# Kernel tuning notes

Hardware: AMD Instinct MI355X
Metric: run time of the kernel (lower is better)

## Reference

```python
import jax, jax.numpy as jnp
import numpy as np

N_TOKENS, D_MODEL, D_FF, N_EXPERTS, TOP_K = 4096, 2048, 1408, 8, 2


def setup_inputs() -> dict:
    key = jax.random.key(0)
    ks = jax.random.split(key, 6)
    s = 0.02
    return {
        "x": jax.random.normal(ks[0], (N_TOKENS, D_MODEL), jnp.float32),
        "topK_indices": jax.random.randint(ks[1], (N_TOKENS, TOP_K), 0, N_EXPERTS, jnp.int32),
        "topK_scores": jax.random.uniform(ks[2], (N_TOKENS, TOP_K), jnp.float32),
        "W_gate": jax.random.normal(ks[3], (N_EXPERTS, D_MODEL, D_FF), jnp.float32) * s,
        "W_up": jax.random.normal(ks[4], (N_EXPERTS, D_MODEL, D_FF), jnp.float32) * s,
        "W_down": jax.random.normal(ks[5], (N_EXPERTS, D_FF, D_MODEL), jnp.float32) * s,
    }


def reference(x, topK_indices, topK_scores, W_gate, W_up, W_down):
    # Combine weights: combine[n, e] = sum over k of score[n, k] where idx[n, k] == e.
    # Mathematically identical to the torch sort/split/index_add dispatch-combine
    # (with multiply_gate_scores=True), expressed densely for a clean jax baseline.
    n = x.shape[0]
    rows = jnp.arange(n)[:, None]  # [N, 1]
    combine = jnp.zeros((n, W_gate.shape[0]), x.dtype).at[rows, topK_indices].add(topK_scores)
    # Per-expert SwiGLU MLP (llama-moe LinearGLUExperts, bias-free).
    h = jax.nn.silu(jnp.einsum("nd,edh->enh", x, W_gate)) * jnp.einsum("nd,edh->enh", x, W_up)
    expert_out = jnp.einsum("enh,ehd->end", h, W_down)  # [E, N, D]
    y = jnp.einsum("ne,end->nd", combine, expert_out)  # weighted scatter-add combine
    return y
```

## Files before the change

kernel.cpp:

```cpp
#include <hip/hip_runtime.h>
#include <hip/hip_bf16.h>


#define NTOK 4096
#define DMODEL 2048
#define DFF 1408
#define NEXP 8
#define TOPK 2
#define NSLOT (NTOK * TOPK)
#define MAX_TILES 160
#define NTILE_A 40
#define NTILE_B 72
#define NY1 11
#define NY2 16

typedef short bf16x8 __attribute__((ext_vector_type(8)));
typedef float f32x4 __attribute__((ext_vector_type(4)));

#define MFMA16(a, b, c) __builtin_amdgcn_mfma_f32_16x16x32_bf16(a, b, c, 0, 0, 0)

__device__ inline void async16(const void* g, void* l) {
    __builtin_amdgcn_global_load_lds(
        (const __attribute__((address_space(1))) void*)g,
        (__attribute__((address_space(3))) void*)l, 16, 0, 0);
}

__device__ inline int xcd_swz(int bid, int nblk) {
    int q = nblk >> 3, r = nblk & 7;
    int x = bid & 7, p = bid >> 3;
    return (x < r ? x * (q + 1) : r * (q + 1) + (x - r) * q) + p;
}

__global__ __launch_bounds__(256) void route_kernel(
    const int* __restrict__ idx, const float* __restrict__ scores,
    int* __restrict__ metaA, int* __restrict__ metaB,
    int* __restrict__ slot_token, float* __restrict__ slot_score,
    int* __restrict__ tok_slot, int bmA, int bmB)
{
    __shared__ int counts[NEXP];
    __shared__ int cursor[NEXP];
    int t = threadIdx.x;
    if (t < NEXP) counts[t] = 0;
    __syncthreads();
    for (int i = t; i < NSLOT; i += 256) atomicAdd(&counts[idx[i]], 1);
    __syncthreads();
    if (t == 0) {
        int off = 0, nt = 0;
        for (int e = 0; e < NEXP; e++) {
            cursor[e] = off;
            int c = counts[e];
            for (int s = 0; s < c && nt < MAX_TILES; s += bmA) {
                metaA[1 + nt * 3 + 0] = e;
                metaA[1 + nt * 3 + 1] = off + s;
                metaA[1 + nt * 3 + 2] = min(bmA, c - s);
                nt++;
            }
            off += c;
        }
        metaA[0] = nt;
        off = 0; nt = 0;
        for (int e = 0; e < NEXP; e++) {
            int c = counts[e];
            for (int s = 0; s < c && nt < MAX_TILES; s += bmB) {
                metaB[1 + nt * 3 + 0] = e;
                metaB[1 + nt * 3 + 1] = off + s;
                metaB[1 + nt * 3 + 2] = min(bmB, c - s);
                nt++;
            }
            off += c;
        }
        metaB[0] = nt;
    }
    __syncthreads();
    for (int i = t; i < NSLOT; i += 256) {
        int e = idx[i];
        int pos = atomicAdd(&cursor[e], 1);
        slot_token[pos] = i / TOPK;
        slot_score[pos] = scores[i];
        tok_slot[i] = pos;
    }
}

__global__ __launch_bounds__(256) void convert_x(
    const float* __restrict__ x, __hip_bfloat16* __restrict__ xb)
{
    int i = blockIdx.x * 256 + threadIdx.x;
    float4 v = reinterpret_cast<const float4*>(x)[i];
    __hip_bfloat16 o[4] = {(__hip_bfloat16)v.x, (__hip_bfloat16)v.y,
                           (__hip_bfloat16)v.z, (__hip_bfloat16)v.w};
    *reinterpret_cast<uint2*>(&xb[(size_t)i * 4]) = *reinterpret_cast<uint2*>(o);
}

__global__ __launch_bounds__(256) void transpose_convert(
    const float* __restrict__ in, __hip_bfloat16* __restrict__ out, int R, int C)
{
    __shared__ __hip_bfloat16 t[64][72];
    const size_t base = (size_t)blockIdx.z * R * C;
    const int c0 = blockIdx.x * 64, r0 = blockIdx.y * 64;
    const int tid = threadIdx.x;
    const int rl = tid >> 4, c4 = (tid & 15) * 4;
    #pragma unroll
    for (int j = 0; j < 4; j++) {
        int r = rl + j * 16;
        float4 v = *reinterpret_cast<const float4*>(&in[base + (size_t)(r0 + r) * C + c0 + c4]);
        t[c4 + 0][r] = (__hip_bfloat16)v.x;
        t[c4 + 1][r] = (__hip_bfloat16)v.y;
        t[c4 + 2][r] = (__hip_bfloat16)v.z;
        t[c4 + 3][r] = (__hip_bfloat16)v.w;
    }
    __syncthreads();
    const int nl = tid >> 3, k8 = (tid & 7) * 8;
    #pragma unroll
    for (int j = 0; j < 2; j++) {
        int n = nl + j * 32;
        const uint* p = reinterpret_cast<const uint*>(&t[n][k8]);
        uint4 o = {p[0], p[1], p[2], p[3]};
        *reinterpret_cast<uint4*>(&out[base + (size_t)(c0 + n) * R + r0 + k8]) = o;
    }
}

__global__ __launch_bounds__(256) void combine_kernel(
    const __hip_bfloat16* __restrict__ so, const int* __restrict__ tok_slot,
    const float* __restrict__ slot_score, float* __restrict__ out)
{
    const int tok = blockIdx.x;
    const int c = threadIdx.x * 8;
    const int s0 = tok_slot[tok * 2 + 0], s1 = tok_slot[tok * 2 + 1];
    const float w0 = slot_score[s0], w1 = slot_score[s1];
    bf16x8 v0 = *reinterpret_cast<const bf16x8*>(&so[(size_t)s0 * DMODEL + c]);
    bf16x8 v1 = *reinterpret_cast<const bf16x8*>(&so[(size_t)s1 * DMODEL + c]);
    float res[8];
    #pragma unroll
    for (int j = 0; j < 8; j++) {
        float f0 = __uint_as_float(((uint)(unsigned short)v0[j]) << 16);
        float f1 = __uint_as_float(((uint)(unsigned short)v1[j]) << 16);
        res[j] = w0 * f0 + w1 * f1;
    }
    float4* dst = reinterpret_cast<float4*>(&out[(size_t)tok * DMODEL + c]);
    dst[0] = *reinterpret_cast<float4*>(&res[0]);
    dst[1] = *reinterpret_cast<float4*>(&res[4]);
}

__global__ __launch_bounds__(512, 2) void moe_gemm1_fast(
    const __hip_bfloat16* __restrict__ xb,
    const __hip_bfloat16* __restrict__ WgT, const __hip_bfloat16* __restrict__ WuT,
    const int* __restrict__ meta, const int* __restrict__ slot_token,
    __hip_bfloat16* __restrict__ h)
{
    const int swz = xcd_swz(blockIdx.x, NTILE_A * NY1);
    const int tile = swz / NY1, yb = swz % NY1;
    if (tile >= meta[0]) return;
    const int e = meta[1 + tile * 3], slot0 = meta[2 + tile * 3], rows = meta[3 + tile * 3];
    const int n0 = yb * 128;

    __shared__ __hip_bfloat16 As[2][256][64];
    __shared__ __hip_bfloat16 Bgs[2][128][64];
    __shared__ __hip_bfloat16 Bus[2][128][64];

    const int tid = threadIdx.x, lane = tid & 63, w = tid >> 6;
    const int wm = w >> 2, wn = w & 3, l15 = lane & 15, lg = lane >> 4;
    const int swb = l15 & 7;

    uint aoff[4], boff[2];
    #pragma unroll
    for (int i = 0; i < 4; i++) {
        int chunk = tid + i * 512;
        int r = chunk >> 3;
        int rc = r < rows ? r : rows - 1;
        int slot8 = (chunk & 7) ^ (r & 7);
        aoff[i] = (uint)(slot_token[slot0 + rc] * (DMODEL * 2) + slot8 * 16);
    }
    #pragma unroll
    for (int i = 0; i < 2; i++) {
        int chunk = tid + i * 512;
        int n = chunk >> 3;
        int slot8 = (chunk & 7) ^ (n & 7);
        boff[i] = (uint)((n0 + n) * (DMODEL * 2) + slot8 * 16);
    }
    const char* xbp = (const char*)xb;
    const char* wgp = (const char*)(WgT + (size_t)e * DFF * DMODEL);
    const char* wup = (const char*)(WuT + (size_t)e * DFF * DMODEL);

    f32x4 ag[8][2] = {};
    f32x4 au[8][2] = {};

    auto stage = [&](int kt, int buf) {
        const int kb = kt * 128;
        char* ab = (char*)As[buf]  + w * 1024;
        char* gb = (char*)Bgs[buf] + w * 1024;
        char* ub = (char*)Bus[buf] + w * 1024;
        #pragma unroll
        for (int i = 0; i < 4; i++) async16(xbp + aoff[i] + kb, ab + i * 8192);
        #pragma unroll
        for (int i = 0; i < 2; i++) {
            async16(wgp + boff[i] + kb, gb + i * 8192);
            async16(wup + boff[i] + kb, ub + i * 8192);
        }
    };

    constexpr int NT = DMODEL / 64;
    stage(0, 0);
    stage(1, 1);

    for (int kt = 0; kt < NT; ++kt) {
        const int cur = kt & 1;
        if (kt < NT - 1) asm volatile("s_waitcnt vmcnt(8)" ::: "memory");
        else             asm volatile("s_waitcnt vmcnt(0)" ::: "memory");
        __builtin_amdgcn_s_barrier();

        bf16x8 bgk[2], buk[2];
        #pragma unroll
        for (int p = 0; p < 4; p++) {
            const int kk = p >> 1, mh = p & 1;
            const int cb = ((kk * 4 + lg) ^ swb) * 16;
            bf16x8 a[4];
            #pragma unroll
            for (int mi = 0; mi < 4; mi++)
                a[mi] = *(const bf16x8*)((const char*)&As[cur][wm * 128 + (mh * 4 + mi) * 16 + l15][0] + cb);
            if (mh == 0) {
                #pragma unroll
                for (int nf = 0; nf < 2; nf++) {
                    bgk[nf] = *(const bf16x8*)((const char*)&Bgs[cur][wn * 32 + nf * 16 + l15][0] + cb);
                    buk[nf] = *(const bf16x8*)((const char*)&Bus[cur][wn * 32 + nf * 16 + l15][0] + cb);
                }
            }
            asm volatile("s_waitcnt lgkmcnt(0)" ::: "memory");
            __builtin_amdgcn_sched_barrier(0);
            __builtin_amdgcn_s_setprio(1);
            #pragma unroll
            for (int mi = 0; mi < 4; mi++) {
                const int mf = mh * 4 + mi;
                #pragma unroll
                for (int nf = 0; nf < 2; nf++) {
                    ag[mf][nf] = MFMA16(a[mi], bgk[nf], ag[mf][nf]);
                    au[mf][nf] = MFMA16(a[mi], buk[nf], au[mf][nf]);
                }
            }
            __builtin_amdgcn_s_setprio(0);
            __builtin_amdgcn_s_barrier();
        }
        if (kt + 2 < NT) stage(kt + 2, cur);
    }

    #pragma unroll
    for (int mf = 0; mf < 8; mf++) {
        #pragma unroll
        for (int j = 0; j < 4; j++) {
            int r = wm * 128 + mf * 16 + lg * 4 + j;
            if (r < rows) {
                size_t hrow = (size_t)(slot0 + r) * DFF + n0 + wn * 32;
                #pragma unroll
                for (int nf = 0; nf < 2; nf++) {
                    float g = ag[mf][nf][j], u = au[mf][nf][j];
                    float hv = g / (1.0f + __expf(-g)) * u;
                    h[hrow + nf * 16 + l15] = (__hip_bfloat16)hv;
                }
            }
        }
    }
}

__global__ __launch_bounds__(256, 2) void moe_gemm2_fast(
    const __hip_bfloat16* __restrict__ h, const __hip_bfloat16* __restrict__ WdT,
    const int* __restrict__ meta, __hip_bfloat16* __restrict__ so)
{
    const int swz = xcd_swz(blockIdx.x, NTILE_B * NY2);
    const int tile = swz / NY2, yb = swz % NY2;
    if (tile >= meta[0]) return;
    const int e = meta[1 + tile * 3], slot0 = meta[2 + tile * 3], rows = meta[3 + tile * 3];
    const int n0 = yb * 128;

    __shared__ __hip_bfloat16 Ah[2][128][64];
    __shared__ __hip_bfloat16 Bd[2][128][64];

    const int tid = threadIdx.x, lane = tid & 63, w = tid >> 6;
    const int wm = w >> 1, wn = w & 1, l15 = lane & 15, lg = lane >> 4;
    const int swb = l15 & 7;

    uint aoff[4], boff[4];
    #pragma unroll
    for (int i = 0; i < 4; i++) {
        int chunk = tid + i * 256;
        int r = chunk >> 3;
        int rc = r < rows ? r : rows - 1;
        int slot8 = (chunk & 7) ^ (r & 7);
        aoff[i] = (uint)((slot0 + rc) * (DFF * 2) + slot8 * 16);
        boff[i] = (uint)((n0 + r) * (DFF * 2) + slot8 * 16);
    }
    const char* hp  = (const char*)h;
    const char* wdp = (const char*)(WdT + (size_t)e * DMODEL * DFF);

    f32x4 acc[4][4] = {};

    auto stage = [&](int kt, int buf) {
        const int kb = kt * 128;
        char* ab = (char*)Ah[buf] + w * 1024;
        char* bb = (char*)Bd[buf] + w * 1024;
        #pragma unroll
        for (int i = 0; i < 4; i++) {
            async16(hp  + aoff[i] + kb, ab + i * 4096);
            async16(wdp + boff[i] + kb, bb + i * 4096);
        }
    };

    constexpr int NT = DFF / 64;
    stage(0, 0);
    stage(1, 1);

    for (int kt = 0; kt < NT; ++kt) {
        const int cur = kt & 1;
        if (kt < NT - 1) asm volatile("s_waitcnt vmcnt(8)" ::: "memory");
        else             asm volatile("s_waitcnt vmcnt(0)" ::: "memory");
        __builtin_amdgcn_s_barrier();

        #pragma unroll
        for (int p = 0; p < 2; p++) {
            const int cb = ((p * 4 + lg) ^ swb) * 16;
            bf16x8 a[4], b[4];
            #pragma unroll
            for (int mf = 0; mf < 4; mf++) {
                a[mf] = *(const bf16x8*)((const char*)&Ah[cur][wm * 64 + mf * 16 + l15][0] + cb);
                b[mf] = *(const bf16x8*)((const char*)&Bd[cur][wn * 64 + mf * 16 + l15][0] + cb);
            }
            asm volatile("s_waitcnt lgkmcnt(0)" ::: "memory");
            __builtin_amdgcn_sched_barrier(0);
            __builtin_amdgcn_s_setprio(1);
            #pragma unroll
            for (int mf = 0; mf < 4; mf++)
                #pragma unroll
                for (int nf = 0; nf < 4; nf++)
                    acc[mf][nf] = MFMA16(a[mf], b[nf], acc[mf][nf]);
            __builtin_amdgcn_s_setprio(0);
            __builtin_amdgcn_s_barrier();
        }
        if (kt + 2 < NT) stage(kt + 2, cur);
    }

    #pragma unroll
    for (int mf = 0; mf < 4; mf++) {
        #pragma unroll
        for (int j = 0; j < 4; j++) {
            int r = wm * 64 + mf * 16 + lg * 4 + j;
            if (r < rows) {
                size_t orow = (size_t)(slot0 + r) * DMODEL + n0 + wn * 64;
                #pragma unroll
                for (int nf = 0; nf < 4; nf++)
                    so[orow + nf * 16 + l15] = (__hip_bfloat16)acc[mf][nf][j];
            }
        }
    }
}

__global__ __launch_bounds__(256) void moe_gemm1(
    const float* __restrict__ x, const float* __restrict__ Wg, const float* __restrict__ Wu,
    const int* __restrict__ meta, const int* __restrict__ slot_token,
    __hip_bfloat16* __restrict__ h)
{
    int tile = blockIdx.x;
    if (tile >= meta[0]) return;
    const int e = meta[1 + tile * 3], slot0 = meta[2 + tile * 3], rows = meta[3 + tile * 3];
    const int n0 = blockIdx.y * 64;
    __shared__ __hip_bfloat16 As[64][72];
    __shared__ __hip_bfloat16 Bgs[64][72];
    __shared__ __hip_bfloat16 Bus[64][72];
    const int tid = threadIdx.x, lane = tid & 63, w = tid >> 6;
    const int wm = w >> 1, wn = w & 1, l15 = lane & 15, lg = lane >> 4;
    const float* __restrict__ WgE = Wg + (size_t)e * DMODEL * DFF;
    const float* __restrict__ WuE = Wu + (size_t)e * DMODEL * DFF;
    f32x4 acc_g[2][2] = {};
    f32x4 acc_u[2][2] = {};
    for (int k0 = 0; k0 < DMODEL; k0 += 64) {
        __syncthreads();
        #pragma unroll
        for (int j = 0; j < 4; j++) {
            int linear = tid + j * 256;
            int r = linear >> 4, c4 = (linear & 15) * 4;
            int tok = (r < rows) ? slot_token[slot0 + r] : 0;
            float4 v = *reinterpret_cast<const float4*>(&x[(size_t)tok * DMODEL + k0 + c4]);
            As[r][c4 + 0] = (__hip_bfloat16)v.x; As[r][c4 + 1] = (__hip_bfloat16)v.y;
            As[r][c4 + 2] = (__hip_bfloat16)v.z; As[r][c4 + 3] = (__hip_bfloat16)v.w;
        }
        #pragma unroll
        for (int j = 0; j < 4; j++) {
            int linear = tid + j * 256;
            int k = linear >> 4, n4 = (linear & 15) * 4;
            float4 vg = *reinterpret_cast<const float4*>(&WgE[(size_t)(k0 + k) * DFF + n0 + n4]);
            Bgs[n4 + 0][k] = (__hip_bfloat16)vg.x; Bgs[n4 + 1][k] = (__hip_bfloat16)vg.y;
            Bgs[n4 + 2][k] = (__hip_bfloat16)vg.z; Bgs[n4 + 3][k] = (__hip_bfloat16)vg.w;
            float4 vu = *reinterpret_cast<const float4*>(&WuE[(size_t)(k0 + k) * DFF + n0 + n4]);
            Bus[n4 + 0][k] = (__hip_bfloat16)vu.x; Bus[n4 + 1][k] = (__hip_bfloat16)vu.y;
            Bus[n4 + 2][k] = (__hip_bfloat16)vu.z; Bus[n4 + 3][k] = (__hip_bfloat16)vu.w;
        }
        __syncthreads();
        #pragma unroll
        for (int kk = 0; kk < 2; kk++) {
            bf16x8 a[2], bg[2], bu[2];
            #pragma unroll
            for (int mf = 0; mf < 2; mf++)
                a[mf] = *reinterpret_cast<const bf16x8*>(&As[wm * 32 + mf * 16 + l15][kk * 32 + lg * 8]);
            #pragma unroll
            for (int nf = 0; nf < 2; nf++) {
                bg[nf] = *reinterpret_cast<const bf16x8*>(&Bgs[wn * 32 + nf * 16 + l15][kk * 32 + lg * 8]);
                bu[nf] = *reinterpret_cast<const bf16x8*>(&Bus[wn * 32 + nf * 16 + l15][kk * 32 + lg * 8]);
            }
            #pragma unroll
            for (int mf = 0; mf < 2; mf++)
                #pragma unroll
                for (int nf = 0; nf < 2; nf++) {
                    acc_g[mf][nf] = MFMA16(a[mf], bg[nf], acc_g[mf][nf]);
                    acc_u[mf][nf] = MFMA16(a[mf], bu[nf], acc_u[mf][nf]);
                }
        }
    }
    #pragma unroll
    for (int mf = 0; mf < 2; mf++)
        #pragma unroll
        for (int nf = 0; nf < 2; nf++)
            #pragma unroll
            for (int j = 0; j < 4; j++) {
                int r = wm * 32 + mf * 16 + lg * 4 + j;
                int c = wn * 32 + nf * 16 + l15;
                if (r < rows) {
                    float g = acc_g[mf][nf][j], u = acc_u[mf][nf][j];
                    h[(size_t)(slot0 + r) * DFF + n0 + c] = (__hip_bfloat16)(g / (1.0f + __expf(-g)) * u);
                }
            }
}

__global__ __launch_bounds__(256) void moe_gemm2(
    const __hip_bfloat16* __restrict__ h, const float* __restrict__ Wd,
    const int* __restrict__ meta, const int* __restrict__ slot_token,
    const float* __restrict__ slot_score, float* __restrict__ out)
{
    int tile = blockIdx.x;
    if (tile >= meta[0]) return;
    const int e = meta[1 + tile * 3], slot0 = meta[2 + tile * 3], rows = meta[3 + tile * 3];
    const int n0 = blockIdx.y * 64;
    __shared__ __hip_bfloat16 As[64][72];
    __shared__ __hip_bfloat16 Bs[64][72];
    const int tid = threadIdx.x, lane = tid & 63, w = tid >> 6;
    const int wm = w >> 1, wn = w & 1, l15 = lane & 15, lg = lane >> 4;
    const float* __restrict__ WdE = Wd + (size_t)e * DFF * DMODEL;
    f32x4 acc[2][2] = {};
    for (int k0 = 0; k0 < DFF; k0 += 64) {
        __syncthreads();
        #pragma unroll
        for (int j = 0; j < 2; j++) {
            int linear = tid + j * 256;
            int r = linear >> 3, c8 = (linear & 7) * 8;
            bf16x8 v = *reinterpret_cast<const bf16x8*>(&h[(size_t)(slot0 + r) * DFF + k0 + c8]);
            *reinterpret_cast<bf16x8*>(&As[r][c8]) = v;
        }
        #pragma unroll
        for (int j = 0; j < 4; j++) {
            int linear = tid + j * 256;
            int k = linear >> 4, n4 = (linear & 15) * 4;
            float4 v = *reinterpret_cast<const float4*>(&WdE[(size_t)(k0 + k) * DMODEL + n0 + n4]);
            Bs[n4 + 0][k] = (__hip_bfloat16)v.x; Bs[n4 + 1][k] = (__hip_bfloat16)v.y;
            Bs[n4 + 2][k] = (__hip_bfloat16)v.z; Bs[n4 + 3][k] = (__hip_bfloat16)v.w;
        }
        __syncthreads();
        #pragma unroll
        for (int kk = 0; kk < 2; kk++) {
            bf16x8 a[2], b[2];
            #pragma unroll
            for (int mf = 0; mf < 2; mf++)
                a[mf] = *reinterpret_cast<const bf16x8*>(&As[wm * 32 + mf * 16 + l15][kk * 32 + lg * 8]);
            #pragma unroll
            for (int nf = 0; nf < 2; nf++)
                b[nf] = *reinterpret_cast<const bf16x8*>(&Bs[wn * 32 + nf * 16 + l15][kk * 32 + lg * 8]);
            #pragma unroll
            for (int mf = 0; mf < 2; mf++)
                #pragma unroll
                for (int nf = 0; nf < 2; nf++)
                    acc[mf][nf] = MFMA16(a[mf], b[nf], acc[mf][nf]);
        }
    }
    #pragma unroll
    for (int mf = 0; mf < 2; mf++)
        #pragma unroll
        for (int nf = 0; nf < 2; nf++)
            #pragma unroll
            for (int j = 0; j < 4; j++) {
                int r = wm * 32 + mf * 16 + lg * 4 + j;
                int c = wn * 32 + nf * 16 + l15;
                if (r < rows) {
                    int slot = slot0 + r;
                    atomicAdd(&out[(size_t)slot_token[slot] * DMODEL + n0 + c],
                              acc[mf][nf][j] * slot_score[slot]);
                }
            }
}

extern "C" void kernel_launch(void* const* d_in, const int* in_sizes, int n_in,
                              void* d_out, int out_size, void* d_ws, size_t ws_size,
                              hipStream_t stream) {
    const float* x      = (const float*)d_in[0];
    const int*   idx    = (const int*)d_in[1];
    const float* scores = (const float*)d_in[2];
    const float* Wg     = (const float*)d_in[3];
    const float* Wu     = (const float*)d_in[4];
    const float* Wd     = (const float*)d_in[5];
    float* out = (float*)d_out;

    char* ws = (char*)d_ws;
    int*   metaA      = (int*)ws;
    int*   metaB      = (int*)(ws + 4096);
    int*   slot_token = (int*)(ws + 8192);
    float* slot_score = (float*)(ws + 8192 + 40960);
    int*   tok_slot   = (int*)(ws + 8192 + 81920);

    const size_t XB_OFF = (size_t)1 << 20;
    const size_t HB_OFF = (size_t)20 << 20;
    const size_t WG_OFF = (size_t)44 << 20;
    const size_t WU_OFF = (size_t)92 << 20;
    const size_t WD_OFF = (size_t)140 << 20;
    const size_t NEED   = (size_t)187 << 20;
    const bool fast = ws_size >= NEED;

    route_kernel<<<1, 256, 0, stream>>>(idx, scores, metaA, metaB, slot_token, slot_score,
                                        tok_slot, fast ? 256 : 64, fast ? 128 : 64);

    if (fast) {
        __hip_bfloat16* xb  = (__hip_bfloat16*)(ws + XB_OFF);
        __hip_bfloat16* hb  = (__hip_bfloat16*)(ws + HB_OFF);
        __hip_bfloat16* WgT = (__hip_bfloat16*)(ws + WG_OFF);
        __hip_bfloat16* WuT = (__hip_bfloat16*)(ws + WU_OFF);
        __hip_bfloat16* WdT = (__hip_bfloat16*)(ws + WD_OFF);
        __hip_bfloat16* sot = (__hip_bfloat16*)(ws + WG_OFF);

        dim3 td(DMODEL / 64, DFF / 64, NEXP);
        transpose_convert<<<td, 256, 0, stream>>>(Wd, WdT, DFF, DMODEL);
        dim3 tg(DFF / 64, DMODEL / 64, NEXP);
        transpose_convert<<<tg, 256, 0, stream>>>(Wg, WgT, DMODEL, DFF);
        transpose_convert<<<tg, 256, 0, stream>>>(Wu, WuT, DMODEL, DFF);
        convert_x<<<(NTOK * DMODEL / 4) / 256, 256, 0, stream>>>(x, xb);

        moe_gemm1_fast<<<NTILE_A * NY1, 512, 0, stream>>>(xb, WgT, WuT, metaA, slot_token, hb);
        moe_gemm2_fast<<<NTILE_B * NY2, 256, 0, stream>>>(hb, WdT, metaB, sot);
        combine_kernel<<<NTOK, 256, 0, stream>>>(sot, tok_slot, slot_score, out);
    } else {
        __hip_bfloat16* hb = (__hip_bfloat16*)(ws + HB_OFF);
        hipMemsetAsync(d_out, 0, (size_t)NTOK * DMODEL * sizeof(float), stream);
        dim3 g1(NSLOT / 64 + NEXP, DFF / 64);
        moe_gemm1<<<g1, 256, 0, stream>>>(x, Wg, Wu, metaA, slot_token, hb);
        dim3 g2(NSLOT / 64 + NEXP, DMODEL / 64);
        moe_gemm2<<<g2, 256, 0, stream>>>(hb, Wd, metaB, slot_token, slot_score, out);
    }
}
```

Before: 364.6 us.

## Restructure MoE GEMM main loops to issue next-stage loads before final MFMAs

In the fused gate/up GEMM, the per-k-tile loop is split into four MFMA phases: gate and up for the first 64 rows, then gate and up for the last 64 rows. The B fragments are kept in registers, and the async global-to-LDS prefetch of tile kt+2 is issued before the final up-projection MFMA batch so that it overlaps with compute. In the down GEMM, all LDS fragments for the tile are loaded at once, the prefetch is issued immediately after a single barrier, and all MFMAs then run. This cuts the barriers per k-tile and overlaps the next stage's loads with compute, at the cost of more fragment registers and changed barrier placement that must keep the LDS double-buffer safe.

```diff
diff --git a/kernel.cpp b/kernel.cpp
--- a/kernel.cpp
+++ b/kernel.cpp
@@ -208,45 +208,91 @@
         else             asm volatile("s_waitcnt vmcnt(0)" ::: "memory");
         __builtin_amdgcn_s_barrier();
 
-        bf16x8 bgk[2], buk[2];
-        #pragma unroll
-        for (int p = 0; p < 4; p++) {
-            const int kk = p >> 1, mh = p & 1;
+        bf16x8 a[4][2], bg[2][2], bu[2][2];
+
+        #pragma unroll
+        for (int kk = 0; kk < 2; kk++) {
             const int cb = ((kk * 4 + lg) ^ swb) * 16;
-            bf16x8 a[4];
             #pragma unroll
             for (int mi = 0; mi < 4; mi++)
-                a[mi] = *(const bf16x8*)((const char*)&As[cur][wm * 128 + (mh * 4 + mi) * 16 + l15][0] + cb);
-            if (mh == 0) {
-                #pragma unroll
-                for (int nf = 0; nf < 2; nf++) {
-                    bgk[nf] = *(const bf16x8*)((const char*)&Bgs[cur][wn * 32 + nf * 16 + l15][0] + cb);
-                    buk[nf] = *(const bf16x8*)((const char*)&Bus[cur][wn * 32 + nf * 16 + l15][0] + cb);
-                }
-            }
-            asm volatile("s_waitcnt lgkmcnt(0)" ::: "memory");
-            __builtin_amdgcn_sched_barrier(0);
-            __builtin_amdgcn_s_setprio(1);
-            #pragma unroll
-            for (int mi = 0; mi < 4; mi++) {
-                const int mf = mh * 4 + mi;
-                #pragma unroll
-                for (int nf = 0; nf < 2; nf++) {
-                    ag[mf][nf] = MFMA16(a[mi], bgk[nf], ag[mf][nf]);
-                    au[mf][nf] = MFMA16(a[mi], buk[nf], au[mf][nf]);
-                }
-            }
-            __builtin_amdgcn_s_setprio(0);
-            __builtin_amdgcn_s_barrier();
-        }
+                a[mi][kk] = *(const bf16x8*)((const char*)&As[cur][wm * 128 + mi * 16 + l15][0] + cb);
+            #pragma unroll
+            for (int nf = 0; nf < 2; nf++)
+                bg[nf][kk] = *(const bf16x8*)((const char*)&Bgs[cur][wn * 32 + nf * 16 + l15][0] + cb);
+        }
+        __builtin_amdgcn_s_barrier();
+        asm volatile("s_waitcnt lgkmcnt(0)" ::: "memory");
+        __builtin_amdgcn_sched_barrier(0);
+        __builtin_amdgcn_s_setprio(1);
+        #pragma unroll
+        for (int kk = 0; kk < 2; kk++)
+            #pragma unroll
+            for (int mi = 0; mi < 4; mi++)
+                #pragma unroll
+                for (int nf = 0; nf < 2; nf++)
+                    ag[mi][nf] = MFMA16(a[mi][kk], bg[nf][kk], ag[mi][nf]);
+        __builtin_amdgcn_s_setprio(0);
+        __builtin_amdgcn_s_barrier();
+
+        #pragma unroll
+        for (int kk = 0; kk < 2; kk++) {
+            const int cb = ((kk * 4 + lg) ^ swb) * 16;
+            #pragma unroll
+            for (int nf = 0; nf < 2; nf++)
+                bu[nf][kk] = *(const bf16x8*)((const char*)&Bus[cur][wn * 32 + nf * 16 + l15][0] + cb);
+        }
+        __builtin_amdgcn_s_barrier();
+        asm volatile("s_waitcnt lgkmcnt(0)" ::: "memory");
+        __builtin_amdgcn_sched_barrier(0);
+        __builtin_amdgcn_s_setprio(1);
+        #pragma unroll
+        for (int kk = 0; kk < 2; kk++)
+            #pragma unroll
+            for (int mi = 0; mi < 4; mi++)
+                #pragma unroll
+                for (int nf = 0; nf < 2; nf++)
+                    au[mi][nf] = MFMA16(a[mi][kk], bu[nf][kk], au[mi][nf]);
+        __builtin_amdgcn_s_setprio(0);
+        __builtin_amdgcn_s_barrier();
+
+        #pragma unroll
+        for (int kk = 0; kk < 2; kk++) {
+            const int cb = ((kk * 4 + lg) ^ swb) * 16;
+            #pragma unroll
+            for (int mi = 0; mi < 4; mi++)
+                a[mi][kk] = *(const bf16x8*)((const char*)&As[cur][wm * 128 + 64 + mi * 16 + l15][0] + cb);
+        }
+        __builtin_amdgcn_s_barrier();
+        asm volatile("s_waitcnt lgkmcnt(0)" ::: "memory");
+        __builtin_amdgcn_sched_barrier(0);
+        __builtin_amdgcn_s_setprio(1);
+        #pragma unroll
+        for (int kk = 0; kk < 2; kk++)
+            #pragma unroll
+            for (int mi = 0; mi < 4; mi++)
+                #pragma unroll
+                for (int nf = 0; nf < 2; nf++)
+                    ag[4 + mi][nf] = MFMA16(a[mi][kk], bg[nf][kk], ag[4 + mi][nf]);
+        __builtin_amdgcn_s_setprio(0);
+        __builtin_amdgcn_s_barrier();
+
         if (kt + 2 < NT) stage(kt + 2, cur);
+        __builtin_amdgcn_s_setprio(1);
+        #pragma unroll
+        for (int kk = 0; kk < 2; kk++)
+            #pragma unroll
+            for (int mi = 0; mi < 4; mi++)
+                #pragma unroll
+                for (int nf = 0; nf < 2; nf++)
+                    au[4 + mi][nf] = MFMA16(a[mi][kk], bu[nf][kk], au[4 + mi][nf]);
+        __builtin_amdgcn_s_setprio(0);
     }
 
     #pragma unroll
     for (int mf = 0; mf < 8; mf++) {
         #pragma unroll
         for (int j = 0; j < 4; j++) {
-            int r = wm * 128 + mf * 16 + lg * 4 + j;
+            int r = wm * 128 + ((mf >> 2) * 64) + (mf & 3) * 16 + lg * 4 + j;
             if (r < rows) {
                 size_t hrow = (size_t)(slot0 + r) * DFF + n0 + wn * 32;
                 #pragma unroll
@@ -313,27 +359,30 @@
         else             asm volatile("s_waitcnt vmcnt(0)" ::: "memory");
         __builtin_amdgcn_s_barrier();
 
-        #pragma unroll
-        for (int p = 0; p < 2; p++) {
-            const int cb = ((p * 4 + lg) ^ swb) * 16;
-            bf16x8 a[4], b[4];
+        bf16x8 a[2][4], b[2][4];
+        #pragma unroll
+        for (int kk = 0; kk < 2; kk++) {
+            const int cb = ((kk * 4 + lg) ^ swb) * 16;
             #pragma unroll
             for (int mf = 0; mf < 4; mf++) {
-                a[mf] = *(const bf16x8*)((const char*)&Ah[cur][wm * 64 + mf * 16 + l15][0] + cb);
-                b[mf] = *(const bf16x8*)((const char*)&Bd[cur][wn * 64 + mf * 16 + l15][0] + cb);
-            }
-            asm volatile("s_waitcnt lgkmcnt(0)" ::: "memory");
-            __builtin_amdgcn_sched_barrier(0);
-            __builtin_amdgcn_s_setprio(1);
+                a[kk][mf] = *(const bf16x8*)((const char*)&Ah[cur][wm * 64 + mf * 16 + l15][0] + cb);
+                b[kk][mf] = *(const bf16x8*)((const char*)&Bd[cur][wn * 64 + mf * 16 + l15][0] + cb);
+            }
+        }
+        asm volatile("s_waitcnt lgkmcnt(0)" ::: "memory");
+        __builtin_amdgcn_sched_barrier(0);
+        __builtin_amdgcn_s_barrier();
+        if (kt + 2 < NT) stage(kt + 2, cur);
+
+        __builtin_amdgcn_s_setprio(1);
+        #pragma unroll
+        for (int kk = 0; kk < 2; kk++)
             #pragma unroll
             for (int mf = 0; mf < 4; mf++)
                 #pragma unroll
                 for (int nf = 0; nf < 4; nf++)
-                    acc[mf][nf] = MFMA16(a[mf], b[nf], acc[mf][nf]);
-            __builtin_amdgcn_s_setprio(0);
-            __builtin_amdgcn_s_barrier();
-        }
-        if (kt + 2 < NT) stage(kt + 2, cur);
+                    acc[mf][nf] = MFMA16(a[kk][mf], b[kk][nf], acc[mf][nf]);
+        __builtin_amdgcn_s_setprio(0);
     }
 
     #pragma unroll
```

Result: faster. 342.5 us (-6.1%).

## Load full K-tile fragments to registers, then issue next-stage prefetch before MFMAs

Applied to the files above, without the earlier changes.

Both expert GEMM kernels now read all LDS fragments for a K-tile into registers up front. After one barrier they issue the async global-to-LDS prefetch for tile kt+2, and only then run the MFMA block. Previously these reads were interleaved across sub-steps with a barrier each, and the prefetch waited until all MFMAs finished. The aim is fewer barriers per tile and earlier prefetch, so global loads overlap compute. The cost is more VGPRs held for fragments, which may reduce occupancy or cause spills, especially in the gate/up kernel.

```diff
diff --git a/kernel.cpp b/kernel.cpp
--- a/kernel.cpp
+++ b/kernel.cpp
@@ -208,38 +208,35 @@
         else             asm volatile("s_waitcnt vmcnt(0)" ::: "memory");
         __builtin_amdgcn_s_barrier();
 
-        bf16x8 bgk[2], buk[2];
-        #pragma unroll
-        for (int p = 0; p < 4; p++) {
-            const int kk = p >> 1, mh = p & 1;
+        bf16x8 a[2][8], bg[2][2], bu[2][2];
+        #pragma unroll
+        for (int kk = 0; kk < 2; kk++) {
             const int cb = ((kk * 4 + lg) ^ swb) * 16;
-            bf16x8 a[4];
-            #pragma unroll
-            for (int mi = 0; mi < 4; mi++)
-                a[mi] = *(const bf16x8*)((const char*)&As[cur][wm * 128 + (mh * 4 + mi) * 16 + l15][0] + cb);
-            if (mh == 0) {
+            #pragma unroll
+            for (int mf = 0; mf < 8; mf++)
+                a[kk][mf] = *(const bf16x8*)((const char*)&As[cur][wm * 128 + mf * 16 + l15][0] + cb);
+            #pragma unroll
+            for (int nf = 0; nf < 2; nf++) {
+                bg[kk][nf] = *(const bf16x8*)((const char*)&Bgs[cur][wn * 32 + nf * 16 + l15][0] + cb);
+                bu[kk][nf] = *(const bf16x8*)((const char*)&Bus[cur][wn * 32 + nf * 16 + l15][0] + cb);
+            }
+        }
+        asm volatile("s_waitcnt lgkmcnt(0)" ::: "memory");
+        __builtin_amdgcn_sched_barrier(0);
+        __builtin_amdgcn_s_barrier();
+        if (kt + 2 < NT) stage(kt + 2, cur);
+
+        __builtin_amdgcn_s_setprio(1);
+        #pragma unroll
+        for (int kk = 0; kk < 2; kk++)
+            #pragma unroll
+            for (int mf = 0; mf < 8; mf++)
                 #pragma unroll
                 for (int nf = 0; nf < 2; nf++) {
-                    bgk[nf] = *(const bf16x8*)((const char*)&Bgs[cur][wn * 32 + nf * 16 + l15][0] + cb);
-                    buk[nf] = *(const bf16x8*)((const char*)&Bus[cur][wn * 32 + nf * 16 + l15][0] + cb);
+                    ag[mf][nf] = MFMA16(a[kk][mf], bg[kk][nf], ag[mf][nf]);
+                    au[mf][nf] = MFMA16(a[kk][mf], bu[kk][nf], au[mf][nf]);
                 }
-            }
-            asm volatile("s_waitcnt lgkmcnt(0)" ::: "memory");
-            __builtin_amdgcn_sched_barrier(0);
-            __builtin_amdgcn_s_setprio(1);
-            #pragma unroll
-            for (int mi = 0; mi < 4; mi++) {
-                const int mf = mh * 4 + mi;
-                #pragma unroll
-                for (int nf = 0; nf < 2; nf++) {
-                    ag[mf][nf] = MFMA16(a[mi], bgk[nf], ag[mf][nf]);
-                    au[mf][nf] = MFMA16(a[mi], buk[nf], au[mf][nf]);
-                }
-            }
-            __builtin_amdgcn_s_setprio(0);
-            __builtin_amdgcn_s_barrier();
-        }
-        if (kt + 2 < NT) stage(kt + 2, cur);
+        __builtin_amdgcn_s_setprio(0);
     }
 
     #pragma unroll
@@ -313,27 +310,30 @@
         else             asm volatile("s_waitcnt vmcnt(0)" ::: "memory");
         __builtin_amdgcn_s_barrier();
 
-        #pragma unroll
-        for (int p = 0; p < 2; p++) {
-            const int cb = ((p * 4 + lg) ^ swb) * 16;
-            bf16x8 a[4], b[4];
+        bf16x8 a[2][4], b[2][4];
+        #pragma unroll
+        for (int kk = 0; kk < 2; kk++) {
+            const int cb = ((kk * 4 + lg) ^ swb) * 16;
             #pragma unroll
             for (int mf = 0; mf < 4; mf++) {
-                a[mf] = *(const bf16x8*)((const char*)&Ah[cur][wm * 64 + mf * 16 + l15][0] + cb);
-                b[mf] = *(const bf16x8*)((const char*)&Bd[cur][wn * 64 + mf * 16 + l15][0] + cb);
-            }
-            asm volatile("s_waitcnt lgkmcnt(0)" ::: "memory");
-            __builtin_amdgcn_sched_barrier(0);
-            __builtin_amdgcn_s_setprio(1);
+                a[kk][mf] = *(const bf16x8*)((const char*)&Ah[cur][wm * 64 + mf * 16 + l15][0] + cb);
+                b[kk][mf] = *(const bf16x8*)((const char*)&Bd[cur][wn * 64 + mf * 16 + l15][0] + cb);
+            }
+        }
+        asm volatile("s_waitcnt lgkmcnt(0)" ::: "memory");
+        __builtin_amdgcn_sched_barrier(0);
+        __builtin_amdgcn_s_barrier();
+        if (kt + 2 < NT) stage(kt + 2, cur);
+
+        __builtin_amdgcn_s_setprio(1);
+        #pragma unroll
+        for (int kk = 0; kk < 2; kk++)
             #pragma unroll
             for (int mf = 0; mf < 4; mf++)
                 #pragma unroll
                 for (int nf = 0; nf < 4; nf++)
-                    acc[mf][nf] = MFMA16(a[mf], b[nf], acc[mf][nf]);
-            __builtin_amdgcn_s_setprio(0);
-            __builtin_amdgcn_s_barrier();
-        }
-        if (kt + 2 < NT) stage(kt + 2, cur);
+                    acc[mf][nf] = MFMA16(a[kk][mf], b[kk][nf], acc[mf][nf]);
+        __builtin_amdgcn_s_setprio(0);
     }
 
     #pragma unroll
```

Result: faster. 324.3 us (median of 2 runs) (-11.0%).

## Shrink MoE GEMM tiles to 128x64 with 32-wide K steps for occupancy

Applied to the files above, without the earlier changes.

Gate/up GEMM moves from 512-thread 256x128 tiles to 256-thread 128x64 tiles that share the 128-row routing metadata with the down GEMM. Both GEMMs now use a K step of 32 with a new 4-way LDS swizzle and issue the next stage right after the LDS reads rather than after compute, aiming at higher occupancy (4 blocks per CU) and better expert-tail balance. The trade-off is lower operand reuse per tile, more global traffic, and twice as many barriers per K. The fallback path also switches its down-GEMM metadata to metaA.

```diff
diff --git a/kernel.cpp b/kernel.cpp
--- a/kernel.cpp
+++ b/kernel.cpp
@@ -9,9 +9,8 @@
 #define TOPK 2
 #define NSLOT (NTOK * TOPK)
 #define MAX_TILES 160
-#define NTILE_A 40
 #define NTILE_B 72
-#define NY1 11
+#define NYG1 22
 #define NY2 16
 
 typedef short bf16x8 __attribute__((ext_vector_type(8)));
@@ -141,112 +140,100 @@
     dst[1] = *reinterpret_cast<float4*>(&res[4]);
 }
 
-__global__ __launch_bounds__(512, 2) void moe_gemm1_fast(
+__global__ __launch_bounds__(256, 4) void moe_gemm1_fast(
     const __hip_bfloat16* __restrict__ xb,
     const __hip_bfloat16* __restrict__ WgT, const __hip_bfloat16* __restrict__ WuT,
     const int* __restrict__ meta, const int* __restrict__ slot_token,
     __hip_bfloat16* __restrict__ h)
 {
-    const int swz = xcd_swz(blockIdx.x, NTILE_A * NY1);
-    const int tile = swz / NY1, yb = swz % NY1;
+    const int swz = xcd_swz(blockIdx.x, NTILE_B * NYG1);
+    const int tile = swz / NYG1, yb = swz % NYG1;
     if (tile >= meta[0]) return;
     const int e = meta[1 + tile * 3], slot0 = meta[2 + tile * 3], rows = meta[3 + tile * 3];
-    const int n0 = yb * 128;
-
-    __shared__ __hip_bfloat16 As[2][256][64];
-    __shared__ __hip_bfloat16 Bgs[2][128][64];
-    __shared__ __hip_bfloat16 Bus[2][128][64];
+    const int n0 = yb * 64;
+
+    __shared__ __hip_bfloat16 As[2][128][32];
+    __shared__ __hip_bfloat16 Bgs[2][64][32];
+    __shared__ __hip_bfloat16 Bus[2][64][32];
 
     const int tid = threadIdx.x, lane = tid & 63, w = tid >> 6;
-    const int wm = w >> 2, wn = w & 3, l15 = lane & 15, lg = lane >> 4;
-    const int swb = l15 & 7;
-
-    uint aoff[4], boff[2];
-    #pragma unroll
-    for (int i = 0; i < 4; i++) {
-        int chunk = tid + i * 512;
-        int r = chunk >> 3;
+    const int wm = w >> 1, wn = w & 1, l15 = lane & 15, lg = lane >> 4;
+
+    uint aoff[2], boff;
+    #pragma unroll
+    for (int i = 0; i < 2; i++) {
+        int c = tid + i * 256;
+        int r = c >> 2;
         int rc = r < rows ? r : rows - 1;
-        int slot8 = (chunk & 7) ^ (r & 7);
-        aoff[i] = (uint)(slot_token[slot0 + rc] * (DMODEL * 2) + slot8 * 16);
-    }
-    #pragma unroll
-    for (int i = 0; i < 2; i++) {
-        int chunk = tid + i * 512;
-        int n = chunk >> 3;
-        int slot8 = (chunk & 7) ^ (n & 7);
-        boff[i] = (uint)((n0 + n) * (DMODEL * 2) + slot8 * 16);
+        int s4 = (c & 3) ^ ((r >> 1) & 3);
+        aoff[i] = (uint)(slot_token[slot0 + rc] * (DMODEL * 2) + s4 * 16);
+    }
+    {
+        int c = tid;
+        int n = c >> 2;
+        int s4 = (c & 3) ^ ((n >> 1) & 3);
+        boff = (uint)((n0 + n) * (DMODEL * 2) + s4 * 16);
     }
     const char* xbp = (const char*)xb;
     const char* wgp = (const char*)(WgT + (size_t)e * DFF * DMODEL);
     const char* wup = (const char*)(WuT + (size_t)e * DFF * DMODEL);
 
-    f32x4 ag[8][2] = {};
-    f32x4 au[8][2] = {};
+    f32x4 ag[4][2] = {};
+    f32x4 au[4][2] = {};
 
     auto stage = [&](int kt, int buf) {
-        const int kb = kt * 128;
+        const int kb = kt * 64;
         char* ab = (char*)As[buf]  + w * 1024;
-        char* gb = (char*)Bgs[buf] + w * 1024;
-        char* ub = (char*)Bus[buf] + w * 1024;
-        #pragma unroll
-        for (int i = 0; i < 4; i++) async16(xbp + aoff[i] + kb, ab + i * 8192);
-        #pragma unroll
-        for (int i = 0; i < 2; i++) {
-            async16(wgp + boff[i] + kb, gb + i * 8192);
-            async16(wup + boff[i] + kb, ub + i * 8192);
-        }
+        async16(xbp + aoff[0] + kb, ab);
+        async16(xbp + aoff[1] + kb, ab + 4096);
+        async16(wgp + boff + kb, (char*)Bgs[buf] + w * 1024);
+        async16(wup + boff + kb, (char*)Bus[buf] + w * 1024);
     };
 
-    constexpr int NT = DMODEL / 64;
+    constexpr int NT = DMODEL / 32;
     stage(0, 0);
     stage(1, 1);
 
     for (int kt = 0; kt < NT; ++kt) {
         const int cur = kt & 1;
-        if (kt < NT - 1) asm volatile("s_waitcnt vmcnt(8)" ::: "memory");
+        if (kt < NT - 1) asm volatile("s_waitcnt vmcnt(4)" ::: "memory");
         else             asm volatile("s_waitcnt vmcnt(0)" ::: "memory");
         __builtin_amdgcn_s_barrier();
 
-        bf16x8 bgk[2], buk[2];
-        #pragma unroll
-        for (int p = 0; p < 4; p++) {
-            const int kk = p >> 1, mh = p & 1;
-            const int cb = ((kk * 4 + lg) ^ swb) * 16;
-            bf16x8 a[4];
-            #pragma unroll
-            for (int mi = 0; mi < 4; mi++)
-                a[mi] = *(const bf16x8*)((const char*)&As[cur][wm * 128 + (mh * 4 + mi) * 16 + l15][0] + cb);
-            if (mh == 0) {
-                #pragma unroll
-                for (int nf = 0; nf < 2; nf++) {
-                    bgk[nf] = *(const bf16x8*)((const char*)&Bgs[cur][wn * 32 + nf * 16 + l15][0] + cb);
-                    buk[nf] = *(const bf16x8*)((const char*)&Bus[cur][wn * 32 + nf * 16 + l15][0] + cb);
-                }
-            }
-            asm volatile("s_waitcnt lgkmcnt(0)" ::: "memory");
-            __builtin_amdgcn_sched_barrier(0);
-            __builtin_amdgcn_s_setprio(1);
-            #pragma unroll
-            for (int mi = 0; mi < 4; mi++) {
-                const int mf = mh * 4 + mi;
-                #pragma unroll
-                for (int nf = 0; nf < 2; nf++) {
-                    ag[mf][nf] = MFMA16(a[mi], bgk[nf], ag[mf][nf]);
-                    au[mf][nf] = MFMA16(a[mi], buk[nf], au[mf][nf]);
-                }
-            }
-            __builtin_amdgcn_s_setprio(0);
-            __builtin_amdgcn_s_barrier();
-        }
+        bf16x8 a[4], bg[2], bu[2];
+        #pragma unroll
+        for (int mf = 0; mf < 4; mf++) {
+            int R = wm * 64 + mf * 16 + l15;
+            a[mf] = *(const bf16x8*)((const char*)&As[cur][R][0] + ((lg ^ ((R >> 1) & 3)) << 4));
+        }
+        #pragma unroll
+        for (int nf = 0; nf < 2; nf++) {
+            int N = wn * 32 + nf * 16 + l15;
+            int cb = (lg ^ ((N >> 1) & 3)) << 4;
+            bg[nf] = *(const bf16x8*)((const char*)&Bgs[cur][N][0] + cb);
+            bu[nf] = *(const bf16x8*)((const char*)&Bus[cur][N][0] + cb);
+        }
+        asm volatile("s_waitcnt lgkmcnt(0)" ::: "memory");
+        __builtin_amdgcn_sched_barrier(0);
+        __builtin_amdgcn_s_barrier();
         if (kt + 2 < NT) stage(kt + 2, cur);
-    }
-
-    #pragma unroll
-    for (int mf = 0; mf < 8; mf++) {
+
+        __builtin_amdgcn_s_setprio(1);
+        #pragma unroll
+        for (int mf = 0; mf < 4; mf++)
+            #pragma unroll
+            for (int nf = 0; nf < 2; nf++) {
+                ag[mf][nf] = MFMA16(a[mf], bg[nf], ag[mf][nf]);
+                au[mf][nf] = MFMA16(a[mf], bu[nf], au[mf][nf]);
+            }
+        __builtin_amdgcn_s_setprio(0);
+    }
+
+    #pragma unroll
+    for (int mf = 0; mf < 4; mf++) {
         #pragma unroll
         for (int j = 0; j < 4; j++) {
-            int r = wm * 128 + mf * 16 + lg * 4 + j;
+            int r = wm * 64 + mf * 16 + lg * 4 + j;
             if (r < rows) {
                 size_t hrow = (size_t)(slot0 + r) * DFF + n0 + wn * 32;
                 #pragma unroll
@@ -260,7 +247,7 @@
     }
 }
 
-__global__ __launch_bounds__(256, 2) void moe_gemm2_fast(
+__global__ __launch_bounds__(256, 4) void moe_gemm2_fast(
     const __hip_bfloat16* __restrict__ h, const __hip_bfloat16* __restrict__ WdT,
     const int* __restrict__ meta, __hip_bfloat16* __restrict__ so)
 {
@@ -270,22 +257,21 @@
     const int e = meta[1 + tile * 3], slot0 = meta[2 + tile * 3], rows = meta[3 + tile * 3];
     const int n0 = yb * 128;
 
-    __shared__ __hip_bfloat16 Ah[2][128][64];
-    __shared__ __hip_bfloat16 Bd[2][128][64];
+    __shared__ __hip_bfloat16 Ah[2][128][32];
+    __shared__ __hip_bfloat16 Bd[2][128][32];
 
     const int tid = threadIdx.x, lane = tid & 63, w = tid >> 6;
     const int wm = w >> 1, wn = w & 1, l15 = lane & 15, lg = lane >> 4;
-    const int swb = l15 & 7;
-
-    uint aoff[4], boff[4];
-    #pragma unroll
-    for (int i = 0; i < 4; i++) {
-        int chunk = tid + i * 256;
-        int r = chunk >> 3;
+
+    uint aoff[2], boff[2];
+    #pragma unroll
+    for (int i = 0; i < 2; i++) {
+        int c = tid + i * 256;
+        int r = c >> 2;
         int rc = r < rows ? r : rows - 1;
-        int slot8 = (chunk & 7) ^ (r & 7);
-        aoff[i] = (uint)((slot0 + rc) * (DFF * 2) + slot8 * 16);
-        boff[i] = (uint)((n0 + r) * (DFF * 2) + slot8 * 16);
+        int s4 = (c & 3) ^ ((r >> 1) & 3);
+        aoff[i] = (uint)((slot0 + rc) * (DFF * 2) + s4 * 16);
+        boff[i] = (uint)((n0 + r) * (DFF * 2) + s4 * 16);
     }
     const char* hp  = (const char*)h;
     const char* wdp = (const char*)(WdT + (size_t)e * DMODEL * DFF);
@@ -293,47 +279,49 @@
     f32x4 acc[4][4] = {};
 
     auto stage = [&](int kt, int buf) {
-        const int kb = kt * 128;
+        const int kb = kt * 64;
         char* ab = (char*)Ah[buf] + w * 1024;
         char* bb = (char*)Bd[buf] + w * 1024;
         #pragma unroll
-        for (int i = 0; i < 4; i++) {
+        for (int i = 0; i < 2; i++) {
             async16(hp  + aoff[i] + kb, ab + i * 4096);
             async16(wdp + boff[i] + kb, bb + i * 4096);
         }
     };
 
-    constexpr int NT = DFF / 64;
+    constexpr int NT = DFF / 32;
     stage(0, 0);
     stage(1, 1);
 
     for (int kt = 0; kt < NT; ++kt) {
         const int cur = kt & 1;
-        if (kt < NT - 1) asm volatile("s_waitcnt vmcnt(8)" ::: "memory");
+        if (kt < NT - 1) asm volatile("s_waitcnt vmcnt(4)" ::: "memory");
         else             asm volatile("s_waitcnt vmcnt(0)" ::: "memory");
         __builtin_amdgcn_s_barrier();
 
-        #pragma unroll
-        for (int p = 0; p < 2; p++) {
-            const int cb = ((p * 4 + lg) ^ swb) * 16;
-            bf16x8 a[4], b[4];
-            #pragma unroll
-            for (int mf = 0; mf < 4; mf++) {
-                a[mf] = *(const bf16x8*)((const char*)&Ah[cur][wm * 64 + mf * 16 + l15][0] + cb);
-                b[mf] = *(const bf16x8*)((const char*)&Bd[cur][wn * 64 + mf * 16 + l15][0] + cb);
-            }
-            asm volatile("s_waitcnt lgkmcnt(0)" ::: "memory");
-            __builtin_amdgcn_sched_barrier(0);
-            __builtin_amdgcn_s_setprio(1);
-            #pragma unroll
-            for (int mf = 0; mf < 4; mf++)
-                #pragma unroll
-                for (int nf = 0; nf < 4; nf++)
-                    acc[mf][nf] = MFMA16(a[mf], b[nf], acc[mf][nf]);
-            __builtin_amdgcn_s_setprio(0);
-            __builtin_amdgcn_s_barrier();
-        }
+        bf16x8 a[4], b[4];
+        #pragma unroll
+        for (int mf = 0; mf < 4; mf++) {
+            int R = wm * 64 + mf * 16 + l15;
+            a[mf] = *(const bf16x8*)((const char*)&Ah[cur][R][0] + ((lg ^ ((R >> 1) & 3)) << 4));
+        }
+        #pragma unroll
+        for (int nf = 0; nf < 4; nf++) {
+            int N = wn * 64 + nf * 16 + l15;
+            b[nf] = *(const bf16x8*)((const char*)&Bd[cur][N][0] + ((lg ^ ((N >> 1) & 3)) << 4));
+        }
+        asm volatile("s_waitcnt lgkmcnt(0)" ::: "memory");
+        __builtin_amdgcn_sched_barrier(0);
+        __builtin_amdgcn_s_barrier();
         if (kt + 2 < NT) stage(kt + 2, cur);
+
+        __builtin_amdgcn_s_setprio(1);
+        #pragma unroll
+        for (int mf = 0; mf < 4; mf++)
+            #pragma unroll
+            for (int nf = 0; nf < 4; nf++)
+                acc[mf][nf] = MFMA16(a[mf], b[nf], acc[mf][nf]);
+        __builtin_amdgcn_s_setprio(0);
     }
 
     #pragma unroll
@@ -519,7 +507,7 @@
     const bool fast = ws_size >= NEED;
 
     route_kernel<<<1, 256, 0, stream>>>(idx, scores, metaA, metaB, slot_token, slot_score,
-                                        tok_slot, fast ? 256 : 64, fast ? 128 : 64);
+                                        tok_slot, 64, fast ? 128 : 64);
 
     if (fast) {
         __hip_bfloat16* xb  = (__hip_bfloat16*)(ws + XB_OFF);
@@ -536,7 +524,7 @@
         transpose_convert<<<tg, 256, 0, stream>>>(Wu, WuT, DMODEL, DFF);
         convert_x<<<(NTOK * DMODEL / 4) / 256, 256, 0, stream>>>(x, xb);
 
-        moe_gemm1_fast<<<NTILE_A * NY1, 512, 0, stream>>>(xb, WgT, WuT, metaA, slot_token, hb);
+        moe_gemm1_fast<<<NTILE_B * NYG1, 256, 0, stream>>>(xb, WgT, WuT, metaB, slot_token, hb);
         moe_gemm2_fast<<<NTILE_B * NY2, 256, 0, stream>>>(hb, WdT, metaB, sot);
         combine_kernel<<<NTOK, 256, 0, stream>>>(sot, tok_slot, slot_score, out);
     } else {
@@ -545,6 +533,6 @@
         dim3 g1(NSLOT / 64 + NEXP, DFF / 64);
         moe_gemm1<<<g1, 256, 0, stream>>>(x, Wg, Wu, metaA, slot_token, hb);
         dim3 g2(NSLOT / 64 + NEXP, DMODEL / 64);
-        moe_gemm2<<<g2, 256, 0, stream>>>(hb, Wd, metaB, slot_token, slot_score, out);
-    }
-}
+        moe_gemm2<<<g2, 256, 0, stream>>>(hb, Wd, metaA, slot_token, slot_score, out);
+    }
+}
```

New measurement: 346.1 us. -5.1%, faster.
